# Kernel tuning notes

Hardware: AMD Instinct MI355X
Metric: run time of the kernel (lower is better)

## Reference

```python
import jax, jax.numpy as jnp
import numpy as np

B, N, F, H = 4, 512, 64, 128
EPS = 0.0            # GINE eps (train_eps=False)
NEG_SLOPE = 0.01     # leaky_relu negative slope


def setup_inputs() -> dict:
    key = jax.random.key(0)
    ks = jax.random.split(key, 8)
    x = jax.random.normal(ks[0], (B, N, F), dtype=jnp.float32)
    adj = jax.random.uniform(ks[1], (B, N, N), dtype=jnp.float32)
    edge_attr = jax.random.normal(ks[2], (B, N, N, F), dtype=jnp.float32)
    mask = jax.random.randint(ks[3], (B, N), 0, 2) > 0  # bool (B,N)
    W1 = jax.random.normal(ks[4], (F, H), dtype=jnp.float32) / np.sqrt(F)
    b1 = jnp.zeros((H,), dtype=jnp.float32)
    W2 = jax.random.normal(ks[5], (H, F), dtype=jnp.float32) / np.sqrt(H)
    b2 = jnp.zeros((F,), dtype=jnp.float32)
    return {"x": x, "adj": adj, "edge_attr": edge_attr, "mask": mask,
            "W1": W1, "b1": b1, "W2": W2, "b2": b2}


def reference(x, adj, edge_attr, mask, W1, b1, W2, b2):
    # z[b,i,j,f] = x[b,i,f] + edge_attr[b,i,j,f]
    # msg = leaky_relu(adj[b,i,j] * z); aggregate over source axis i (dim 1)
    msg = jax.nn.leaky_relu(adj[..., None] * (x[:, :, None, :] + edge_attr),
                            negative_slope=NEG_SLOPE)
    agg = jnp.sum(msg, axis=1)                      # (B, N, F), indexed by j
    out = (1.0 + EPS) * x + agg                     # add_loop=True
    # nn applied on masked rows, zeros elsewhere (equivalent to out[mask]=nn(out[mask]))
    h = jax.nn.leaky_relu(out @ W1 + b1, negative_slope=NEG_SLOPE) @ W2 + b2
    return jnp.where(mask[..., None], h, jnp.zeros((), dtype=h.dtype))
```

## Files before the change

### kernel.cpp

```cpp
#include <hip/hip_runtime.h>


namespace {

constexpr int Bc = 4;
constexpr int Nc = 512;
constexpr int Fc = 64;
constexpr int Hc = 128;
constexpr float NEG = 0.01f;

__device__ __forceinline__ float lrelu(float z) {
  return z > 0.f ? z : z * NEG;
}

__global__ __launch_bounds__(256) void gine_fused(
    const float* __restrict__ x,
    const float* __restrict__ adj,
    const float* __restrict__ ea,
    const int* __restrict__ mask,
    const float* __restrict__ W1,
    const float* __restrict__ b1,
    const float* __restrict__ W2,
    const float* __restrict__ b2,
    float* __restrict__ out)
{
  const int blk = blockIdx.x;
  const int b = blk >> 9;
  const int j = blk & (Nc - 1);
  const int tid = threadIdx.x;
  const int f4 = tid & 15;
  const int ip = tid >> 4;

  __shared__ float s_adj[Nc];
  __shared__ float4 s_part[256];
  __shared__ float s_out[Fc];
  __shared__ float s_hid[Hc];

  const float* adjb = adj + b * Nc * Nc;
  s_adj[tid]       = adjb[tid * Nc + j];
  s_adj[tid + 256] = adjb[(tid + 256) * Nc + j];
  __syncthreads();

  const float4* xb  = reinterpret_cast<const float4*>(x + b * Nc * Fc);
  const float4* eab = reinterpret_cast<const float4*>(ea) +
                      ((b * Nc) * Nc + j) * (Fc / 4);

  float4 acc = make_float4(0.f, 0.f, 0.f, 0.f);
  #pragma unroll 4
  for (int i = ip; i < Nc; i += 16) {
    const float a = s_adj[i];
    const float4 xv = xb[i * (Fc / 4) + f4];
    const float4 ev = eab[i * (Nc * Fc / 4) + f4];
    acc.x += lrelu(a * (xv.x + ev.x));
    acc.y += lrelu(a * (xv.y + ev.y));
    acc.z += lrelu(a * (xv.z + ev.z));
    acc.w += lrelu(a * (xv.w + ev.w));
  }

  s_part[tid] = acc;
  __syncthreads();
  #pragma unroll
  for (int s = 128; s >= 16; s >>= 1) {
    if (tid < s) {
      float4 p = s_part[tid];
      const float4 q = s_part[tid + s];
      p.x += q.x; p.y += q.y; p.z += q.z; p.w += q.w;
      s_part[tid] = p;
    }
    __syncthreads();
  }

  if (tid < 16) {
    float4 r = s_part[tid];
    const float4 xj = xb[j * (Fc / 4) + tid];
    r.x += xj.x; r.y += xj.y; r.z += xj.z; r.w += xj.w;
    reinterpret_cast<float4*>(s_out)[tid] = r;
  }
  __syncthreads();

  if (tid < Hc) {
    float h = b1[tid];
    #pragma unroll
    for (int f = 0; f < Fc; ++f)
      h = fmaf(s_out[f], W1[f * Hc + tid], h);
    s_hid[tid] = lrelu(h);
  }
  __syncthreads();

  if (tid < Fc) {
    float o = b2[tid];
    #pragma unroll
    for (int h = 0; h < Hc; ++h)
      o = fmaf(s_hid[h], W2[h * Fc + tid], o);
    const int row = b * Nc + j;
    out[row * Fc + tid] = (mask[row] != 0) ? o : 0.f;
  }
}

}

extern "C" void kernel_launch(void* const* d_in, const int* in_sizes, int n_in,
                              void* d_out, int out_size, void* d_ws, size_t ws_size,
                              hipStream_t stream) {
  const float* x    = (const float*)d_in[0];
  const float* adj  = (const float*)d_in[1];
  const float* ea   = (const float*)d_in[2];
  const int*   mask = (const int*)d_in[3];
  const float* W1   = (const float*)d_in[4];
  const float* b1   = (const float*)d_in[5];
  const float* W2   = (const float*)d_in[6];
  const float* b2   = (const float*)d_in[7];
  float* out = (float*)d_out;

  gine_fused<<<dim3(Bc * Nc), dim3(256), 0, stream>>>(
      x, adj, ea, mask, W1, b1, W2, b2, out);
}
```

Before: 380.9 us.

## Process four destination nodes per block with 512 threads

Each block now handles four consecutive j columns. This allows float4 loads of adj rows, contiguous 1 KB edge_attr reads per source i, and reuse of x rows and the MLP weights across four outputs. The block count drops to 512 and the block size grows to 512 threads, with the reduction and MLP stages re-indexed per row. The intent is better coalescing and amortised weight loads in a bandwidth-bound kernel. The cost is fewer blocks and higher shared memory use per block.

```diff
diff --git a/kernel.cpp b/kernel.cpp
--- a/kernel.cpp
+++ b/kernel.cpp
@@ -7,13 +7,15 @@
 constexpr int Nc = 512;
 constexpr int Fc = 64;
 constexpr int Hc = 128;
+constexpr int TJ = 4;
+constexpr int TH = 512;
 constexpr float NEG = 0.01f;
 
 __device__ __forceinline__ float lrelu(float z) {
   return z > 0.f ? z : z * NEG;
 }
 
-__global__ __launch_bounds__(256) void gine_fused(
+__global__ __launch_bounds__(TH, 4) void gine_fused(
     const float* __restrict__ x,
     const float* __restrict__ adj,
     const float* __restrict__ ea,
@@ -25,32 +27,33 @@
     float* __restrict__ out)
 {
   const int blk = blockIdx.x;
-  const int b = blk >> 9;
-  const int j = blk & (Nc - 1);
+  const int b   = blk >> 7;
+  const int j0  = (blk & 127) * TJ;
   const int tid = threadIdx.x;
-  const int f4 = tid & 15;
-  const int ip = tid >> 4;
+  const int f4  = tid & 15;
+  const int jl  = (tid >> 4) & 3;
+  const int ip  = tid >> 6;
 
-  __shared__ float s_adj[Nc];
-  __shared__ float4 s_part[256];
-  __shared__ float s_out[Fc];
-  __shared__ float s_hid[Hc];
+  __shared__ float4 s_adj4[Nc];
+  __shared__ float4 s_part[TH];
+  __shared__ float  s_out[TJ][Fc];
+  __shared__ float  s_hid[TJ][Hc];
 
-  const float* adjb = adj + b * Nc * Nc;
-  s_adj[tid]       = adjb[tid * Nc + j];
-  s_adj[tid + 256] = adjb[(tid + 256) * Nc + j];
+  const float* adjb = adj + (size_t)b * Nc * Nc;
+  s_adj4[tid] = *reinterpret_cast<const float4*>(adjb + (size_t)tid * Nc + j0);
   __syncthreads();
 
-  const float4* xb  = reinterpret_cast<const float4*>(x + b * Nc * Fc);
-  const float4* eab = reinterpret_cast<const float4*>(ea) +
-                      ((b * Nc) * Nc + j) * (Fc / 4);
+  const float4* xb4 = reinterpret_cast<const float4*>(x + (size_t)b * Nc * Fc);
+  const float4* eap = reinterpret_cast<const float4*>(ea)
+                    + ((size_t)b * Nc * Nc + (j0 + jl)) * (Fc / 4) + f4;
+  constexpr int ISTRIDE = Nc * Fc / 4;
 
   float4 acc = make_float4(0.f, 0.f, 0.f, 0.f);
   #pragma unroll 4
-  for (int i = ip; i < Nc; i += 16) {
-    const float a = s_adj[i];
-    const float4 xv = xb[i * (Fc / 4) + f4];
-    const float4 ev = eab[i * (Nc * Fc / 4) + f4];
+  for (int i = ip; i < Nc; i += 8) {
+    const float a   = reinterpret_cast<const float*>(&s_adj4[i])[jl];
+    const float4 xv = xb4[i * (Fc / 4) + f4];
+    const float4 ev = eap[(size_t)i * ISTRIDE];
     acc.x += lrelu(a * (xv.x + ev.x));
     acc.y += lrelu(a * (xv.y + ev.y));
     acc.z += lrelu(a * (xv.z + ev.z));
@@ -60,7 +63,7 @@
   s_part[tid] = acc;
   __syncthreads();
   #pragma unroll
-  for (int s = 128; s >= 16; s >>= 1) {
+  for (int s = 256; s >= 64; s >>= 1) {
     if (tid < s) {
       float4 p = s_part[tid];
       const float4 q = s_part[tid + s];
@@ -70,30 +73,36 @@
     __syncthreads();
   }
 
-  if (tid < 16) {
+  if (tid < 64) {
+    const int row = tid >> 4;
+    const int fg  = tid & 15;
     float4 r = s_part[tid];
-    const float4 xj = xb[j * (Fc / 4) + tid];
+    const float4 xj = xb4[(j0 + row) * (Fc / 4) + fg];
     r.x += xj.x; r.y += xj.y; r.z += xj.z; r.w += xj.w;
-    reinterpret_cast<float4*>(s_out)[tid] = r;
+    reinterpret_cast<float4*>(&s_out[row][0])[fg] = r;
   }
   __syncthreads();
 
-  if (tid < Hc) {
-    float h = b1[tid];
-    #pragma unroll
+  {
+    const int row = tid >> 7;
+    const int h   = tid & 127;
+    float hv = b1[h];
+    #pragma unroll 8
     for (int f = 0; f < Fc; ++f)
-      h = fmaf(s_out[f], W1[f * Hc + tid], h);
-    s_hid[tid] = lrelu(h);
+      hv = fmaf(s_out[row][f], W1[f * Hc + h], hv);
+    s_hid[row][h] = lrelu(hv);
   }
   __syncthreads();
 
-  if (tid < Fc) {
-    float o = b2[tid];
-    #pragma unroll
+  if (tid < TJ * Fc) {
+    const int row = tid >> 6;
+    const int f   = tid & 63;
+    float o = b2[f];
+    #pragma unroll 8
     for (int h = 0; h < Hc; ++h)
-      o = fmaf(s_hid[h], W2[h * Fc + tid], o);
-    const int row = b * Nc + j;
-    out[row * Fc + tid] = (mask[row] != 0) ? o : 0.f;
+      o = fmaf(s_hid[row][h], W2[h * Fc + f], o);
+    const int rowg = b * Nc + j0 + row;
+    out[rowg * Fc + f] = (mask[rowg] != 0) ? o : 0.f;
   }
 }
 
@@ -112,6 +121,6 @@
   const float* b2   = (const float*)d_in[7];
   float* out = (float*)d_out;
 
-  gine_fused<<<dim3(Bc * Nc), dim3(256), 0, stream>>>(
+  gine_fused<<<dim3(Bc * Nc / TJ), dim3(TH), 0, stream>>>(
       x, adj, ea, mask, W1, b1, W2, b2, out);
 }
```

Measured after the change: 378.8 us, median of 2. Within noise of the previous version (-0.6%).
